# Performance work log

Hardware: AMD Instinct MI355X
Metric: run time of the kernel (lower is better)

## Reference

```python
import jax, jax.numpy as jnp
import numpy as np

N_NODES = 30000
N_EDGES = 150000
N_REL = 10
IN_DIM = 256
OUT_DIM = 256


def setup_inputs() -> dict:
    key = jax.random.key(0)
    ks = jax.random.split(key, 10)
    s = 1.0 / np.sqrt(IN_DIM)  # ~nn.Linear init scale
    return {
        "x": jax.random.normal(ks[0], (N_NODES, IN_DIM), jnp.float32),
        "W_self": jax.random.uniform(ks[1], (IN_DIM, OUT_DIM), jnp.float32, -s, s),
        "b_self": jax.random.uniform(ks[2], (OUT_DIM,), jnp.float32, -s, s),
        "W_fwd": jax.random.uniform(ks[3], (N_REL, IN_DIM, OUT_DIM), jnp.float32, -s, s),
        "b_fwd": jax.random.uniform(ks[4], (N_REL, OUT_DIM), jnp.float32, -s, s),
        "W_rev": jax.random.uniform(ks[5], (N_REL, IN_DIM, OUT_DIM), jnp.float32, -s, s),
        "b_rev": jax.random.uniform(ks[6], (N_REL, OUT_DIM), jnp.float32, -s, s),
        "dep_idx": jax.random.randint(ks[7], (N_EDGES,), 0, N_NODES, jnp.int32),
        "rel_idx": jax.random.randint(ks[8], (N_EDGES,), 0, N_REL, jnp.int32),
        "gov_idx": jax.random.randint(ks[9], (N_EDGES,), 0, N_NODES, jnp.int32),
    }


def reference(x, W_self, b_self, W_fwd, b_fwd, W_rev, b_rev, dep_idx, rel_idx, gov_idx):
    # self transform for every token: [N, out]
    out = x @ W_self + b_self
    # transform all nodes by every relation weight up-front: [R, N, out]
    H_fwd = jnp.einsum("ni,rio->rno", x, W_fwd) + b_fwd[:, None, :]
    H_rev = jnp.einsum("ni,rio->rno", x, W_rev) + b_rev[:, None, :]
    # per-edge gather: forward msg uses governor feature, reverse msg uses dependent
    msg_fwd = H_fwd[rel_idx, gov_idx]  # [E, out]
    msg_rev = H_rev[rel_idx, dep_idx]  # [E, out]
    # scatter-add: forward msg -> dependent, reverse msg -> governor
    out = out.at[dep_idx].add(msg_fwd)
    out = out.at[gov_idx].add(msg_rev)
    return out
```

## Files before the change

kernel.cpp:

```cpp
#include <hip/hip_runtime.h>

#define N_NODES 30000
#define N_EDGES 150000
#define N_REL 10
#define DIM 256

#define SORT_BLOCKS 120
#define SORT_CHUNK ((N_EDGES + SORT_BLOCKS - 1) / SORT_BLOCKS)

#define SCAN_CHUNK 256
#define SCAN_BLOCKS ((N_NODES + SCAN_CHUNK - 1) / SCAN_CHUNK)

#define A_STRIDE 280

#define PREP_XB 7500
#define PREP_WB 5376
#define PREP_ZB 235

typedef __attribute__((ext_vector_type(8))) short bf16x8;
typedef __attribute__((ext_vector_type(4))) float f32x4;

__device__ __forceinline__ unsigned short f2bf(float f) {
  union { float f; unsigned int u; } v; v.f = f;
  unsigned int u = v.u;
  unsigned int r = u + 0x7fffu + ((u >> 16) & 1u);
  return (unsigned short)(r >> 16);
}


__global__ void prep_kernel(const float* __restrict__ x,
                            const float* __restrict__ Wf,
                            const float* __restrict__ Wr,
                            const float* __restrict__ Ws,
                            unsigned short* __restrict__ xbf,
                            unsigned short* __restrict__ wt,
                            int* __restrict__ cnt) {
  int b = blockIdx.x;
  if (b < PREP_XB) {
    int idx = b * 256 + threadIdx.x;
    float4 v = reinterpret_cast<const float4*>(x)[idx];
    ushort4 o;
    o.x = f2bf(v.x); o.y = f2bf(v.y); o.z = f2bf(v.z); o.w = f2bf(v.w);
    reinterpret_cast<ushort4*>(xbf)[idx] = o;
  } else if (b < PREP_XB + PREP_WB) {
    int idx = (b - PREP_XB) * 256 + threadIdx.x;
    int bb = idx >> 16;
    int t = idx & 65535;
    int o = t >> 8, i = t & 255;
    const float* src = (bb < N_REL) ? (Wf + (size_t)bb * 65536)
                     : (bb < 2 * N_REL) ? (Wr + (size_t)(bb - N_REL) * 65536)
                     : Ws;
    wt[idx] = f2bf(src[i * 256 + o]);
  } else {
    int i = (b - PREP_XB - PREP_WB) * 256 + threadIdx.x;
    if (i < 2 * N_NODES) cnt[i] = 0;
  }
}

__global__ void hist_all_kernel(const int* __restrict__ rel,
                                const int* __restrict__ dep,
                                const int* __restrict__ gov,
                                int* __restrict__ block_counts,
                                int* __restrict__ cnt) {
  __shared__ int h[N_REL];
  if (threadIdx.x < N_REL) h[threadIdx.x] = 0;
  __syncthreads();
  int beg = blockIdx.x * SORT_CHUNK;
  int end = min(beg + SORT_CHUNK, N_EDGES);
  for (int e = beg + threadIdx.x; e < end; e += blockDim.x) {
    atomicAdd(&h[rel[e]], 1);
    atomicAdd(&cnt[dep[e]], 1);
    atomicAdd(&cnt[N_NODES + gov[e]], 1);
  }
  __syncthreads();
  if (threadIdx.x < N_REL)
    block_counts[blockIdx.x * N_REL + threadIdx.x] = h[threadIdx.x];
}

__global__ void scan_rel_kernel(const int* __restrict__ block_counts,
                                int* __restrict__ rel_start,
                                int* __restrict__ block_offset) {
  __shared__ int tot[N_REL];
  int r = threadIdx.x;
  if (r < N_REL) {
    int s = 0;
    for (int b = 0; b < SORT_BLOCKS; ++b) s += block_counts[b * N_REL + r];
    tot[r] = s;
  }
  __syncthreads();
  if (threadIdx.x == 0) {
    int s = 0;
    for (int i = 0; i < N_REL; ++i) { rel_start[i] = s; s += tot[i]; }
    rel_start[N_REL] = s;
  }
  __syncthreads();
  if (r < N_REL) {
    int run = rel_start[r];
    for (int b = 0; b < SORT_BLOCKS; ++b) {
      block_offset[b * N_REL + r] = run;
      run += block_counts[b * N_REL + r];
    }
  }
}

__global__ void scanA_kernel(const int* __restrict__ cnt,
                             int* __restrict__ tmp, int* __restrict__ sums) {
  __shared__ int s[SCAN_CHUNK];
  int d = blockIdx.y, b = blockIdx.x, t = threadIdx.x;
  int i = b * SCAN_CHUNK + t;
  int v = (i < N_NODES) ? cnt[d * N_NODES + i] : 0;
  s[t] = v;
  __syncthreads();
  for (int off = 1; off < SCAN_CHUNK; off <<= 1) {
    int add = (t >= off) ? s[t - off] : 0;
    __syncthreads();
    s[t] += add;
    __syncthreads();
  }
  if (i < N_NODES) tmp[d * N_NODES + i] = s[t] - v;
  if (t == SCAN_CHUNK - 1) sums[d * SCAN_BLOCKS + b] = s[t];
}

__global__ void scanB_kernel(const int* __restrict__ sums,
                             int* __restrict__ chunk_off, int* __restrict__ rp) {
  __shared__ int s[128];
  int d = blockIdx.x, t = threadIdx.x;
  int v = (t < SCAN_BLOCKS) ? sums[d * SCAN_BLOCKS + t] : 0;
  s[t] = v;
  __syncthreads();
  for (int off = 1; off < 128; off <<= 1) {
    int add = (t >= off) ? s[t - off] : 0;
    __syncthreads();
    s[t] += add;
    __syncthreads();
  }
  if (t < SCAN_BLOCKS) chunk_off[d * SCAN_BLOCKS + t] = s[t] - v;
  if (t == 127) rp[d * (N_NODES + 1) + N_NODES] = s[127];
}

__global__ void scanC_kernel(const int* __restrict__ tmp,
                             const int* __restrict__ chunk_off,
                             int* __restrict__ rp, int* __restrict__ cursor) {
  int d = blockIdx.y;
  int i = blockIdx.x * SCAN_CHUNK + threadIdx.x;
  if (i < N_NODES) {
    int v = tmp[d * N_NODES + i] + chunk_off[d * SCAN_BLOCKS + blockIdx.x];
    rp[d * (N_NODES + 1) + i] = v;
    cursor[d * N_NODES + i] = v;
  }
}

__global__ void scatter_all_kernel(const int* __restrict__ rel,
                                   const int* __restrict__ dep,
                                   const int* __restrict__ gov,
                                   const int* __restrict__ block_offset,
                                   int* __restrict__ cursor,
                                   int* __restrict__ perm,
                                   int* __restrict__ colf,
                                   int* __restrict__ colr) {
  __shared__ int cur[N_REL];
  if (threadIdx.x < N_REL)
    cur[threadIdx.x] = block_offset[blockIdx.x * N_REL + threadIdx.x];
  __syncthreads();
  int beg = blockIdx.x * SORT_CHUNK;
  int end = min(beg + SORT_CHUNK, N_EDGES);
  for (int e = beg + threadIdx.x; e < end; e += blockDim.x) {
    int pos = atomicAdd(&cur[rel[e]], 1);
    perm[pos] = e;
    colf[atomicAdd(&cursor[dep[e]], 1)] = pos;
    colr[atomicAdd(&cursor[N_NODES + gov[e]], 1)] = pos;
  }
}


__global__ __launch_bounds__(256, 2)
void mega_gemm_kernel(const unsigned short* __restrict__ xbf,
                      const unsigned short* __restrict__ wt,
                      const float* __restrict__ b_self,
                      const float* __restrict__ b_fwd,
                      const float* __restrict__ b_rev,
                      const int* __restrict__ perm,
                      const int* __restrict__ rel_start,
                      const int* __restrict__ dep,
                      const int* __restrict__ gov,
                      unsigned short* __restrict__ msg,
                      float* __restrict__ out) {
  const int bkt = blockIdx.y;
  const bool is_self = (bkt == 2 * N_REL);
  const int r = bkt % N_REL;
  const bool fwd = bkt < N_REL;

  int beg, cnt;
  const int* src_idx = fwd ? gov : dep;
  unsigned short* mdir = msg + (fwd ? 0 : (size_t)N_EDGES * DIM);
  if (is_self) { beg = 0; cnt = N_NODES; }
  else { beg = rel_start[r]; cnt = rel_start[r + 1] - beg; }
  const int ntiles = (cnt + 63) >> 6;

  const int tid = threadIdx.x;
  const int wave = tid >> 6, lane = tid & 63;
  const int lm = lane & 15, q = lane >> 4;
  const int nb = wave * 64;

  __shared__ int s_src[64];
  __shared__ unsigned short sA[64 * A_STRIDE];

  bf16x8 wf[8][4];
  const unsigned short* wbase = wt + (size_t)bkt * DIM * DIM;
  #pragma unroll
  for (int kk = 0; kk < 8; ++kk)
    #pragma unroll
    for (int ni = 0; ni < 4; ++ni)
      wf[kk][ni] = *reinterpret_cast<const bf16x8*>(
          wbase + (size_t)(nb + ni * 16 + lm) * DIM + kk * 32 + q * 8);

  const float* bptr = is_self ? b_self : ((fwd ? b_fwd : b_rev) + r * DIM);
  float bias[4];
  #pragma unroll
  for (int ni = 0; ni < 4; ++ni) bias[ni] = bptr[nb + ni * 16 + lm];

  for (int t = blockIdx.x; t < ntiles; t += gridDim.x) {
    const int tile0 = t << 6;
    const int rows_valid = min(64, cnt - tile0);

    if (tid < 64) {
      int s;
      if (is_self) {
        int rr = tile0 + tid;
        s = rr < N_NODES ? rr : N_NODES - 1;
      } else {
        s = (tid < rows_valid) ? src_idx[perm[beg + tile0 + tid]] : 0;
      }
      s_src[tid] = s;
    }
    __syncthreads();

    {
      int half = lane >> 5;
      int lcol = lane & 31;
      #pragma unroll
      for (int i = 0; i < 8; ++i) {
        int row = wave * 16 + i * 2 + half;
        uint4 v = *reinterpret_cast<const uint4*>(
            xbf + (size_t)s_src[row] * DIM + lcol * 8);
        *reinterpret_cast<uint4*>(sA + row * A_STRIDE + lcol * 8) = v;
      }
    }
    __syncthreads();

    f32x4 acc[4][4];
    #pragma unroll
    for (int mi = 0; mi < 4; ++mi)
      #pragma unroll
      for (int ni = 0; ni < 4; ++ni)
        acc[mi][ni] = (f32x4){0.f, 0.f, 0.f, 0.f};

    #pragma unroll
    for (int kk = 0; kk < 8; ++kk) {
      bf16x8 a[4];
      #pragma unroll
      for (int mi = 0; mi < 4; ++mi)
        a[mi] = *reinterpret_cast<const bf16x8*>(
            sA + (mi * 16 + lm) * A_STRIDE + kk * 32 + q * 8);
      #pragma unroll
      for (int mi = 0; mi < 4; ++mi)
        #pragma unroll
        for (int ni = 0; ni < 4; ++ni)
          acc[mi][ni] = __builtin_amdgcn_mfma_f32_16x16x32_bf16(a[mi], wf[kk][ni], acc[mi][ni], 0, 0, 0);
    }

    if (is_self) {
      #pragma unroll
      for (int mi = 0; mi < 4; ++mi) {
        #pragma unroll
        for (int reg = 0; reg < 4; ++reg) {
          int row = mi * 16 + q * 4 + reg;
          if (row < rows_valid) {
            #pragma unroll
            for (int ni = 0; ni < 4; ++ni)
              out[(size_t)(tile0 + row) * DIM + nb + ni * 16 + lm] =
                  acc[mi][ni][reg] + bias[ni];
          }
        }
      }
    } else {
      #pragma unroll
      for (int mi = 0; mi < 4; ++mi) {
        #pragma unroll
        for (int reg = 0; reg < 4; ++reg) {
          int row = mi * 16 + q * 4 + reg;
          if (row < rows_valid) {
            unsigned int p0 = ((unsigned int)f2bf(acc[mi][1][reg] + bias[1]) << 16) |
                              f2bf(acc[mi][0][reg] + bias[0]);
            unsigned int p1 = ((unsigned int)f2bf(acc[mi][3][reg] + bias[3]) << 16) |
                              f2bf(acc[mi][2][reg] + bias[2]);
            uint2 u; u.x = p0; u.y = p1;
            *reinterpret_cast<uint2*>(
                mdir + (size_t)(beg + tile0 + row) * DIM + nb + lm * 4) = u;
          }
        }
      }
    }
    __syncthreads();
  }
}


__global__ void reduce_both_kernel(const unsigned short* __restrict__ msg,
                                   const int* __restrict__ rp,
                                   const int* __restrict__ colf,
                                   const int* __restrict__ colr,
                                   float* __restrict__ out) {
  const int n = blockIdx.x, t = threadIdx.x;
  const int g = t >> 6, lane = t & 63;
  const int b0 = rp[n], e0 = rp[n + 1];
  const int b1 = rp[(N_NODES + 1) + n], e1 = rp[(N_NODES + 1) + n + 1];
  if (e0 <= b0 && e1 <= b1) return;

  float a0 = 0.f, a1 = 0.f, a2 = 0.f, a3 = 0.f;
  for (int j = b0 + g; j < e0; j += 4) {
    int row = colf[j];
    uint2 v = *reinterpret_cast<const uint2*>(msg + (size_t)row * DIM + lane * 4);
    union { unsigned int u; float f; } c;
    c.u = v.x << 16;          a0 += c.f;
    c.u = v.x & 0xffff0000u;  a1 += c.f;
    c.u = v.y << 16;          a2 += c.f;
    c.u = v.y & 0xffff0000u;  a3 += c.f;
  }
  for (int j = b1 + g; j < e1; j += 4) {
    int row = colr[j];
    uint2 v = *reinterpret_cast<const uint2*>(
        msg + (size_t)(N_EDGES + row) * DIM + lane * 4);
    union { unsigned int u; float f; } c;
    c.u = v.x << 16;          a0 += c.f;
    c.u = v.x & 0xffff0000u;  a1 += c.f;
    c.u = v.y << 16;          a2 += c.f;
    c.u = v.y & 0xffff0000u;  a3 += c.f;
  }

  __shared__ float part[4][DIM];
  const int cb = (lane >> 4) * 64 + (lane & 15);
  part[g][cb +  0] = a0;
  part[g][cb + 16] = a1;
  part[g][cb + 32] = a2;
  part[g][cb + 48] = a3;
  __syncthreads();
  float s = part[0][t] + part[1][t] + part[2][t] + part[3][t];
  out[(size_t)n * DIM + t] += s;
}


__global__ __launch_bounds__(256, 2)
void self_gemm_kernel(const unsigned short* __restrict__ xbf,
                      const unsigned short* __restrict__ wt_self,
                      const float* __restrict__ b_self,
                      float* __restrict__ out) {
  const int tid = threadIdx.x;
  const int wave = tid >> 6, lane = tid & 63;
  const int lm = lane & 15, q = lane >> 4;
  const int nb = wave * 64;

  bf16x8 wf[8][4];
  #pragma unroll
  for (int kk = 0; kk < 8; ++kk)
    #pragma unroll
    for (int ni = 0; ni < 4; ++ni)
      wf[kk][ni] = *reinterpret_cast<const bf16x8*>(
          wt_self + (size_t)(nb + ni * 16 + lm) * DIM + kk * 32 + q * 8);

  float bias[4];
  #pragma unroll
  for (int ni = 0; ni < 4; ++ni) bias[ni] = b_self[nb + ni * 16 + lm];

  const int ntiles = (N_NODES + 63) / 64;
  for (int t = blockIdx.x; t < ntiles; t += gridDim.x) {
    const int row0 = t * 64;
    const unsigned short* xr[4];
    #pragma unroll
    for (int mi = 0; mi < 4; ++mi) {
      int r = row0 + mi * 16 + lm;
      int rc = r < N_NODES ? r : N_NODES - 1;
      xr[mi] = xbf + (size_t)rc * DIM + q * 8;
    }

    f32x4 acc[4][4];
    #pragma unroll
    for (int mi = 0; mi < 4; ++mi)
      #pragma unroll
      for (int ni = 0; ni < 4; ++ni)
        acc[mi][ni] = (f32x4){0.f, 0.f, 0.f, 0.f};

    #pragma unroll
    for (int kk = 0; kk < 8; ++kk) {
      bf16x8 a[4];
      #pragma unroll
      for (int mi = 0; mi < 4; ++mi)
        a[mi] = *reinterpret_cast<const bf16x8*>(xr[mi] + kk * 32);
      #pragma unroll
      for (int mi = 0; mi < 4; ++mi)
        #pragma unroll
        for (int ni = 0; ni < 4; ++ni)
          acc[mi][ni] = __builtin_amdgcn_mfma_f32_16x16x32_bf16(a[mi], wf[kk][ni], acc[mi][ni], 0, 0, 0);
    }

    #pragma unroll
    for (int mi = 0; mi < 4; ++mi) {
      #pragma unroll
      for (int reg = 0; reg < 4; ++reg) {
        int row = row0 + mi * 16 + q * 4 + reg;
        if (row < N_NODES) {
          #pragma unroll
          for (int ni = 0; ni < 4; ++ni)
            out[(size_t)row * DIM + nb + ni * 16 + lm] = acc[mi][ni][reg] + bias[ni];
        }
      }
    }
  }
}

__global__ void edge_gemm_atomic_kernel(const unsigned short* __restrict__ xbf,
                                        const unsigned short* __restrict__ wt,
                                        const float* __restrict__ b_fwd,
                                        const float* __restrict__ b_rev,
                                        const int* __restrict__ perm,
                                        const int* __restrict__ rel_start,
                                        const int* __restrict__ dep,
                                        const int* __restrict__ gov,
                                        float* __restrict__ out) {
  const int bucket = blockIdx.y;
  const int r = bucket % N_REL;
  const bool fwd = bucket < N_REL;
  const int beg = rel_start[r];
  const int cnt = rel_start[r + 1] - beg;
  const int ntiles = (cnt + 63) >> 6;

  const int tid = threadIdx.x;
  const int wave = tid >> 6, lane = tid & 63;
  const int lm = lane & 15, q = lane >> 4;
  const int nb = wave * 64;

  __shared__ int s_src[64], s_dst[64];

  const unsigned short* wr[4];
  #pragma unroll
  for (int ni = 0; ni < 4; ++ni)
    wr[ni] = wt + (size_t)bucket * DIM * DIM + (size_t)(nb + ni * 16 + lm) * DIM + q * 8;

  const float* bptr = (fwd ? b_fwd : b_rev) + r * DIM;
  float bias[4];
  #pragma unroll
  for (int ni = 0; ni < 4; ++ni) bias[ni] = bptr[nb + ni * 16 + lm];

  for (int t = blockIdx.x; t < ntiles; t += gridDim.x) {
    const int tile0 = t << 6;
    const int rows_valid = min(64, cnt - tile0);

    if (tid < 64) {
      int s = 0, d = -1;
      if (tid < rows_valid) {
        int e = perm[beg + tile0 + tid];
        int gv = gov[e], dp = dep[e];
        s = fwd ? gv : dp;
        d = fwd ? dp : gv;
      }
      s_src[tid] = s;
      s_dst[tid] = d;
    }
    __syncthreads();

    const unsigned short* xr[4];
    #pragma unroll
    for (int mi = 0; mi < 4; ++mi)
      xr[mi] = xbf + (size_t)s_src[mi * 16 + lm] * DIM + q * 8;

    f32x4 acc[4][4];
    #pragma unroll
    for (int mi = 0; mi < 4; ++mi)
      #pragma unroll
      for (int ni = 0; ni < 4; ++ni)
        acc[mi][ni] = (f32x4){0.f, 0.f, 0.f, 0.f};

    #pragma unroll
    for (int k0 = 0; k0 < DIM; k0 += 32) {
      bf16x8 a[4], b[4];
      #pragma unroll
      for (int mi = 0; mi < 4; ++mi) a[mi] = *reinterpret_cast<const bf16x8*>(xr[mi] + k0);
      #pragma unroll
      for (int ni = 0; ni < 4; ++ni) b[ni] = *reinterpret_cast<const bf16x8*>(wr[ni] + k0);
      #pragma unroll
      for (int mi = 0; mi < 4; ++mi)
        #pragma unroll
        for (int ni = 0; ni < 4; ++ni)
          acc[mi][ni] = __builtin_amdgcn_mfma_f32_16x16x32_bf16(a[mi], b[ni], acc[mi][ni], 0, 0, 0);
    }

    #pragma unroll
    for (int mi = 0; mi < 4; ++mi) {
      #pragma unroll
      for (int reg = 0; reg < 4; ++reg) {
        int row = mi * 16 + q * 4 + reg;
        if (row < rows_valid) {
          int dst = s_dst[row];
          float* op = out + (size_t)dst * DIM + nb + lm;
          #pragma unroll
          for (int ni = 0; ni < 4; ++ni)
            atomicAdd(op + ni * 16, acc[mi][ni][reg] + bias[ni]);
        }
      }
    }
    __syncthreads();
  }
}


extern "C" void kernel_launch(void* const* d_in, const int* in_sizes, int n_in,
                              void* d_out, int out_size, void* d_ws, size_t ws_size,
                              hipStream_t stream) {
  const float* x      = (const float*)d_in[0];
  const float* W_self = (const float*)d_in[1];
  const float* b_self = (const float*)d_in[2];
  const float* W_fwd  = (const float*)d_in[3];
  const float* b_fwd  = (const float*)d_in[4];
  const float* W_rev  = (const float*)d_in[5];
  const float* b_rev  = (const float*)d_in[6];
  const int* dep = (const int*)d_in[7];
  const int* rel = (const int*)d_in[8];
  const int* gov = (const int*)d_in[9];
  float* out = (float*)d_out;

  char* base = (char*)d_ws;
  size_t off = 0;
  auto alloc = [&](size_t bytes) -> char* {
    char* p = base + off;
    off = (off + bytes + 15) & ~(size_t)15;
    return p;
  };

  unsigned short* xbf = (unsigned short*)alloc((size_t)N_NODES * DIM * 2);
  unsigned short* wt  = (unsigned short*)alloc((size_t)21 * DIM * DIM * 2);
  int* perm          = (int*)alloc((size_t)N_EDGES * 4);
  int* rel_start     = (int*)alloc(16 * 4);
  int* block_counts  = (int*)alloc(SORT_BLOCKS * N_REL * 4);
  int* block_offset  = (int*)alloc(SORT_BLOCKS * N_REL * 4);
  int* cnt       = (int*)alloc((size_t)2 * N_NODES * 4);
  int* tmp       = (int*)alloc((size_t)2 * N_NODES * 4);
  int* sums      = (int*)alloc((size_t)2 * SCAN_BLOCKS * 4);
  int* chunk_off = (int*)alloc((size_t)2 * SCAN_BLOCKS * 4);
  int* rp        = (int*)alloc((size_t)2 * (N_NODES + 1) * 4);
  int* cursor    = (int*)alloc((size_t)2 * N_NODES * 4);
  int* colf      = (int*)alloc((size_t)N_EDGES * 4);
  int* colr      = (int*)alloc((size_t)N_EDGES * 4);
  unsigned short* msg = (unsigned short*)alloc((size_t)2 * N_EDGES * DIM * 2);
  const bool two_phase = (off <= ws_size);

  prep_kernel<<<PREP_XB + PREP_WB + PREP_ZB, 256, 0, stream>>>(
      x, W_fwd, W_rev, W_self, xbf, wt, cnt);
  hist_all_kernel<<<SORT_BLOCKS, 256, 0, stream>>>(rel, dep, gov, block_counts, cnt);
  scan_rel_kernel<<<1, 64, 0, stream>>>(block_counts, rel_start, block_offset);
  scanA_kernel<<<dim3(SCAN_BLOCKS, 2), SCAN_CHUNK, 0, stream>>>(cnt, tmp, sums);
  scanB_kernel<<<2, 128, 0, stream>>>(sums, chunk_off, rp);
  scanC_kernel<<<dim3(SCAN_BLOCKS, 2), SCAN_CHUNK, 0, stream>>>(tmp, chunk_off, rp, cursor);
  scatter_all_kernel<<<SORT_BLOCKS, 256, 0, stream>>>(
      rel, dep, gov, block_offset, cursor, perm, colf, colr);

  if (two_phase) {
    mega_gemm_kernel<<<dim3(48, 2 * N_REL + 1), 256, 0, stream>>>(
        xbf, wt, b_self, b_fwd, b_rev, perm, rel_start, dep, gov, msg, out);
    reduce_both_kernel<<<N_NODES, 256, 0, stream>>>(msg, rp, colf, colr, out);
  } else {
    self_gemm_kernel<<<120, 256, 0, stream>>>(
        xbf, wt + (size_t)20 * DIM * DIM, b_self, out);
    edge_gemm_atomic_kernel<<<dim3(260, 20), 256, 0, stream>>>(
        xbf, wt, b_fwd, b_rev, perm, rel_start, dep, gov, out);
  }
}
```

Before: 280.9 us.

## Merge forward/reverse CSR into one adjacency and fuse scans into one kernel

Builds a single combined CSR per destination node, where forward entries store the message row and reverse entries store N_EDGES plus the row. The three-kernel two-pass scan and the separate relation scan are replaced by one two-block kernel that scans both. The reduce kernel walks one list with eight half-wave groups doing 16-byte loads instead of two lists with four groups. This removes several kernel launches and widens the gather loads. The cost is a serial single-block scan of 30000 counts and more shared-memory partials in the reduce.

```diff
diff --git a/kernel.cpp b/kernel.cpp
--- a/kernel.cpp
+++ b/kernel.cpp
@@ -8,14 +8,11 @@
 #define SORT_BLOCKS 120
 #define SORT_CHUNK ((N_EDGES + SORT_BLOCKS - 1) / SORT_BLOCKS)
 
-#define SCAN_CHUNK 256
-#define SCAN_BLOCKS ((N_NODES + SCAN_CHUNK - 1) / SCAN_CHUNK)
-
 #define A_STRIDE 280
 
 #define PREP_XB 7500
 #define PREP_WB 5376
-#define PREP_ZB 235
+#define PREP_ZB 118
 
 typedef __attribute__((ext_vector_type(8))) short bf16x8;
 typedef __attribute__((ext_vector_type(4))) float f32x4;
@@ -53,7 +50,7 @@
     wt[idx] = f2bf(src[i * 256 + o]);
   } else {
     int i = (b - PREP_XB - PREP_WB) * 256 + threadIdx.x;
-    if (i < 2 * N_NODES) cnt[i] = 0;
+    if (i < N_NODES) cnt[i] = 0;
   }
 }
 
@@ -70,83 +67,65 @@
   for (int e = beg + threadIdx.x; e < end; e += blockDim.x) {
     atomicAdd(&h[rel[e]], 1);
     atomicAdd(&cnt[dep[e]], 1);
-    atomicAdd(&cnt[N_NODES + gov[e]], 1);
+    atomicAdd(&cnt[gov[e]], 1);
   }
   __syncthreads();
   if (threadIdx.x < N_REL)
     block_counts[blockIdx.x * N_REL + threadIdx.x] = h[threadIdx.x];
 }
 
-__global__ void scan_rel_kernel(const int* __restrict__ block_counts,
-                                int* __restrict__ rel_start,
-                                int* __restrict__ block_offset) {
-  __shared__ int tot[N_REL];
-  int r = threadIdx.x;
-  if (r < N_REL) {
+__global__ void scan_fused_kernel(const int* __restrict__ block_counts,
+                                  const int* __restrict__ cnt,
+                                  int* __restrict__ rel_start,
+                                  int* __restrict__ block_offset,
+                                  int* __restrict__ rp,
+                                  int* __restrict__ cursor) {
+  if (blockIdx.x == 0) {
+    __shared__ int tot[N_REL];
+    int r = threadIdx.x;
+    if (r < N_REL) {
+      int s = 0;
+      for (int b = 0; b < SORT_BLOCKS; ++b) s += block_counts[b * N_REL + r];
+      tot[r] = s;
+    }
+    __syncthreads();
+    if (threadIdx.x == 0) {
+      int s = 0;
+      for (int i = 0; i < N_REL; ++i) { rel_start[i] = s; s += tot[i]; }
+      rel_start[N_REL] = s;
+    }
+    __syncthreads();
+    if (r < N_REL) {
+      int run = rel_start[r];
+      for (int b = 0; b < SORT_BLOCKS; ++b) {
+        block_offset[b * N_REL + r] = run;
+        run += block_counts[b * N_REL + r];
+      }
+    }
+  } else {
+    __shared__ int part[256];
+    const int CH = (N_NODES + 255) / 256;
+    int t = threadIdx.x;
+    int b0 = t * CH;
     int s = 0;
-    for (int b = 0; b < SORT_BLOCKS; ++b) s += block_counts[b * N_REL + r];
-    tot[r] = s;
-  }
-  __syncthreads();
-  if (threadIdx.x == 0) {
-    int s = 0;
-    for (int i = 0; i < N_REL; ++i) { rel_start[i] = s; s += tot[i]; }
-    rel_start[N_REL] = s;
-  }
-  __syncthreads();
-  if (r < N_REL) {
-    int run = rel_start[r];
-    for (int b = 0; b < SORT_BLOCKS; ++b) {
-      block_offset[b * N_REL + r] = run;
-      run += block_counts[b * N_REL + r];
-    }
-  }
-}
-
-__global__ void scanA_kernel(const int* __restrict__ cnt,
-                             int* __restrict__ tmp, int* __restrict__ sums) {
-  __shared__ int s[SCAN_CHUNK];
-  int d = blockIdx.y, b = blockIdx.x, t = threadIdx.x;
-  int i = b * SCAN_CHUNK + t;
-  int v = (i < N_NODES) ? cnt[d * N_NODES + i] : 0;
-  s[t] = v;
-  __syncthreads();
-  for (int off = 1; off < SCAN_CHUNK; off <<= 1) {
-    int add = (t >= off) ? s[t - off] : 0;
-    __syncthreads();
-    s[t] += add;
-    __syncthreads();
-  }
-  if (i < N_NODES) tmp[d * N_NODES + i] = s[t] - v;
-  if (t == SCAN_CHUNK - 1) sums[d * SCAN_BLOCKS + b] = s[t];
-}
-
-__global__ void scanB_kernel(const int* __restrict__ sums,
-                             int* __restrict__ chunk_off, int* __restrict__ rp) {
-  __shared__ int s[128];
-  int d = blockIdx.x, t = threadIdx.x;
-  int v = (t < SCAN_BLOCKS) ? sums[d * SCAN_BLOCKS + t] : 0;
-  s[t] = v;
-  __syncthreads();
-  for (int off = 1; off < 128; off <<= 1) {
-    int add = (t >= off) ? s[t - off] : 0;
-    __syncthreads();
-    s[t] += add;
-    __syncthreads();
-  }
-  if (t < SCAN_BLOCKS) chunk_off[d * SCAN_BLOCKS + t] = s[t] - v;
-  if (t == 127) rp[d * (N_NODES + 1) + N_NODES] = s[127];
-}
-
-__global__ void scanC_kernel(const int* __restrict__ tmp,
-                             const int* __restrict__ chunk_off,
-                             int* __restrict__ rp, int* __restrict__ cursor) {
-  int d = blockIdx.y;
-  int i = blockIdx.x * SCAN_CHUNK + threadIdx.x;
-  if (i < N_NODES) {
-    int v = tmp[d * N_NODES + i] + chunk_off[d * SCAN_BLOCKS + blockIdx.x];
-    rp[d * (N_NODES + 1) + i] = v;
-    cursor[d * N_NODES + i] = v;
+    for (int i = 0; i < CH; ++i) {
+      int j = b0 + i;
+      if (j < N_NODES) s += cnt[j];
+    }
+    part[t] = s;
+    __syncthreads();
+    for (int off = 1; off < 256; off <<= 1) {
+      int add = (t >= off) ? part[t - off] : 0;
+      __syncthreads();
+      part[t] += add;
+      __syncthreads();
+    }
+    int run = (t == 0) ? 0 : part[t - 1];
+    for (int i = 0; i < CH; ++i) {
+      int j = b0 + i;
+      if (j < N_NODES) { rp[j] = run; cursor[j] = run; run += cnt[j]; }
+    }
+    if (t == 255) rp[N_NODES] = run;
   }
 }
 
@@ -156,8 +135,7 @@
                                    const int* __restrict__ block_offset,
                                    int* __restrict__ cursor,
                                    int* __restrict__ perm,
-                                   int* __restrict__ colf,
-                                   int* __restrict__ colr) {
+                                   int* __restrict__ col) {
   __shared__ int cur[N_REL];
   if (threadIdx.x < N_REL)
     cur[threadIdx.x] = block_offset[blockIdx.x * N_REL + threadIdx.x];
@@ -167,8 +145,8 @@
   for (int e = beg + threadIdx.x; e < end; e += blockDim.x) {
     int pos = atomicAdd(&cur[rel[e]], 1);
     perm[pos] = e;
-    colf[atomicAdd(&cursor[dep[e]], 1)] = pos;
-    colr[atomicAdd(&cursor[N_NODES + gov[e]], 1)] = pos;
+    col[atomicAdd(&cursor[dep[e]], 1)] = pos;
+    col[atomicAdd(&cursor[gov[e]], 1)] = N_EDGES + pos;
   }
 }
 
@@ -306,46 +284,47 @@
 }
 
 
-__global__ void reduce_both_kernel(const unsigned short* __restrict__ msg,
-                                   const int* __restrict__ rp,
-                                   const int* __restrict__ colf,
-                                   const int* __restrict__ colr,
-                                   float* __restrict__ out) {
+__global__ void reduce_kernel(const unsigned short* __restrict__ msg,
+                              const int* __restrict__ rp,
+                              const int* __restrict__ col,
+                              float* __restrict__ out) {
   const int n = blockIdx.x, t = threadIdx.x;
   const int g = t >> 6, lane = t & 63;
-  const int b0 = rp[n], e0 = rp[n + 1];
-  const int b1 = rp[(N_NODES + 1) + n], e1 = rp[(N_NODES + 1) + n + 1];
-  if (e0 <= b0 && e1 <= b1) return;
-
-  float a0 = 0.f, a1 = 0.f, a2 = 0.f, a3 = 0.f;
-  for (int j = b0 + g; j < e0; j += 4) {
-    int row = colf[j];
-    uint2 v = *reinterpret_cast<const uint2*>(msg + (size_t)row * DIM + lane * 4);
+  const int half = lane >> 5, l = lane & 31;
+  const int grp = g * 2 + half;
+  const int beg = rp[n], end = rp[n + 1];
+  if (end <= beg) return;
+
+  float a[8];
+  #pragma unroll
+  for (int k = 0; k < 8; ++k) a[k] = 0.f;
+
+  for (int j = beg + grp; j < end; j += 8) {
+    int row = col[j];
+    uint4 v = *reinterpret_cast<const uint4*>(msg + (size_t)row * DIM + l * 8);
     union { unsigned int u; float f; } c;
-    c.u = v.x << 16;          a0 += c.f;
-    c.u = v.x & 0xffff0000u;  a1 += c.f;
-    c.u = v.y << 16;          a2 += c.f;
-    c.u = v.y & 0xffff0000u;  a3 += c.f;
-  }
-  for (int j = b1 + g; j < e1; j += 4) {
-    int row = colr[j];
-    uint2 v = *reinterpret_cast<const uint2*>(
-        msg + (size_t)(N_EDGES + row) * DIM + lane * 4);
-    union { unsigned int u; float f; } c;
-    c.u = v.x << 16;          a0 += c.f;
-    c.u = v.x & 0xffff0000u;  a1 += c.f;
-    c.u = v.y << 16;          a2 += c.f;
-    c.u = v.y & 0xffff0000u;  a3 += c.f;
-  }
-
-  __shared__ float part[4][DIM];
-  const int cb = (lane >> 4) * 64 + (lane & 15);
-  part[g][cb +  0] = a0;
-  part[g][cb + 16] = a1;
-  part[g][cb + 32] = a2;
-  part[g][cb + 48] = a3;
+    c.u = v.x << 16;          a[0] += c.f;
+    c.u = v.x & 0xffff0000u;  a[1] += c.f;
+    c.u = v.y << 16;          a[2] += c.f;
+    c.u = v.y & 0xffff0000u;  a[3] += c.f;
+    c.u = v.z << 16;          a[4] += c.f;
+    c.u = v.z & 0xffff0000u;  a[5] += c.f;
+    c.u = v.w << 16;          a[6] += c.f;
+    c.u = v.w & 0xffff0000u;  a[7] += c.f;
+  }
+
+  __shared__ float part[8][DIM];
+  const int nb = (l >> 3) << 6;
+  #pragma unroll
+  for (int k = 0; k < 8; ++k) {
+    int lm = (l & 7) * 2 + (k >> 2);
+    int i = k & 3;
+    part[grp][nb + i * 16 + lm] = a[k];
+  }
   __syncthreads();
-  float s = part[0][t] + part[1][t] + part[2][t] + part[3][t];
+  float s = 0.f;
+  #pragma unroll
+  for (int k = 0; k < 8; ++k) s += part[k][t];
   out[(size_t)n * DIM + t] += s;
 }
 
@@ -542,31 +521,25 @@
   int* rel_start     = (int*)alloc(16 * 4);
   int* block_counts  = (int*)alloc(SORT_BLOCKS * N_REL * 4);
   int* block_offset  = (int*)alloc(SORT_BLOCKS * N_REL * 4);
-  int* cnt       = (int*)alloc((size_t)2 * N_NODES * 4);
-  int* tmp       = (int*)alloc((size_t)2 * N_NODES * 4);
-  int* sums      = (int*)alloc((size_t)2 * SCAN_BLOCKS * 4);
-  int* chunk_off = (int*)alloc((size_t)2 * SCAN_BLOCKS * 4);
-  int* rp        = (int*)alloc((size_t)2 * (N_NODES + 1) * 4);
-  int* cursor    = (int*)alloc((size_t)2 * N_NODES * 4);
-  int* colf      = (int*)alloc((size_t)N_EDGES * 4);
-  int* colr      = (int*)alloc((size_t)N_EDGES * 4);
+  int* cnt    = (int*)alloc((size_t)N_NODES * 4);
+  int* rp     = (int*)alloc((size_t)(N_NODES + 1) * 4);
+  int* cursor = (int*)alloc((size_t)N_NODES * 4);
+  int* col    = (int*)alloc((size_t)2 * N_EDGES * 4);
   unsigned short* msg = (unsigned short*)alloc((size_t)2 * N_EDGES * DIM * 2);
   const bool two_phase = (off <= ws_size);
 
   prep_kernel<<<PREP_XB + PREP_WB + PREP_ZB, 256, 0, stream>>>(
       x, W_fwd, W_rev, W_self, xbf, wt, cnt);
   hist_all_kernel<<<SORT_BLOCKS, 256, 0, stream>>>(rel, dep, gov, block_counts, cnt);
-  scan_rel_kernel<<<1, 64, 0, stream>>>(block_counts, rel_start, block_offset);
-  scanA_kernel<<<dim3(SCAN_BLOCKS, 2), SCAN_CHUNK, 0, stream>>>(cnt, tmp, sums);
-  scanB_kernel<<<2, 128, 0, stream>>>(sums, chunk_off, rp);
-  scanC_kernel<<<dim3(SCAN_BLOCKS, 2), SCAN_CHUNK, 0, stream>>>(tmp, chunk_off, rp, cursor);
+  scan_fused_kernel<<<2, 256, 0, stream>>>(
+      block_counts, cnt, rel_start, block_offset, rp, cursor);
   scatter_all_kernel<<<SORT_BLOCKS, 256, 0, stream>>>(
-      rel, dep, gov, block_offset, cursor, perm, colf, colr);
+      rel, dep, gov, block_offset, cursor, perm, col);
 
   if (two_phase) {
     mega_gemm_kernel<<<dim3(48, 2 * N_REL + 1), 256, 0, stream>>>(
         xbf, wt, b_self, b_fwd, b_rev, perm, rel_start, dep, gov, msg, out);
-    reduce_both_kernel<<<N_NODES, 256, 0, stream>>>(msg, rp, colf, colr, out);
+    reduce_kernel<<<N_NODES, 256, 0, stream>>>(msg, rp, col, out);
   } else {
     self_gemm_kernel<<<120, 256, 0, stream>>>(
         xbf, wt + (size_t)20 * DIM * DIM, b_self, out);
```

Result: slower. 336.6 us (+19.8%).
